# Performance work log

Hardware: AMD Instinct MI355X
Metric: run time of the kernel (lower is better)

## Reference

```python
import jax, jax.numpy as jnp
import numpy as np

N_NODES = 50000


def gcn_conv(x, W, b, src, dst, n_nodes):
    """PyG GCNConv: x' = D^-1/2 (A+I) D^-1/2 (x W) + b (symmetric norm, self-loops)."""
    h = x @ W  # [N, out]
    loop = jnp.arange(n_nodes, dtype=src.dtype)
    src_f = jnp.concatenate([src, loop])
    dst_f = jnp.concatenate([dst, loop])
    ones = jnp.ones(src_f.shape[0], dtype=h.dtype)
    deg = jax.ops.segment_sum(ones, dst_f, num_segments=n_nodes)
    dinv = jnp.where(deg > 0, jax.lax.rsqrt(deg), 0.0)
    norm = dinv[src_f] * dinv[dst_f]  # [E+N]
    msg = h[src_f] * norm[:, None]    # irregular gather over edges
    out = jax.ops.segment_sum(msg, dst_f, num_segments=n_nodes)
    return out + b


def setup_inputs() -> dict:
    key = jax.random.key(0)
    ks = jax.random.split(key, 9)
    d_in, d_h = 128, 128
    x = jax.random.normal(ks[0], (N_NODES, d_in), dtype=jnp.float32)
    edge_index = jax.random.randint(ks[1], (2, 800000), 0, N_NODES, dtype=jnp.int64)
    glorot = lambda k, fi, fo: jax.random.normal(k, (fi, fo), dtype=jnp.float32) * jnp.sqrt(2.0 / (fi + fo))
    return {
        "x": x,
        "edge_index": edge_index,
        "W1": glorot(ks[2], d_in, d_h), "b1": jnp.zeros((d_h,), jnp.float32),
        "W2": glorot(ks[3], d_h, d_h), "b2": jnp.zeros((d_h,), jnp.float32),
        "W3": glorot(ks[4], d_h, d_h), "b3": jnp.zeros((d_h,), jnp.float32),
    }


def reference(x, edge_index, W1, b1, W2, b2, W3, b3):
    src, dst = edge_index[0], edge_index[1]
    n = x.shape[0]
    h = jax.nn.relu(gcn_conv(x, W1, b1, src, dst, n))
    h = jax.nn.relu(gcn_conv(h, W2, b2, src, dst, n))
    h = gcn_conv(h, W3, b3, src, dst, n)
    return h
```

## Files before the change

kernel.cpp:

```cpp
#include <hip/hip_runtime.h>

#define N_NODES 50000
#define N_EDGES 800000
#define DIM 128
#define WT_BLOCKS 192
#define GEMM_BLOCKS ((N_NODES + 127) / 128)
#define NBUCKET ((N_NODES + 255) / 256)
#define P1_BLOCKS 200
#define P1_CHUNK 4000
#define P2_BLOCKS 200
#define P2_CHUNK 4000

typedef unsigned int u32;
typedef short bf16x8 __attribute__((ext_vector_type(8)));
typedef float f32x4 __attribute__((ext_vector_type(4)));

static inline size_t alignUp(size_t x) { return (x + 255) & ~size_t(255); }

__device__ inline unsigned short f2bf(float f) {
    union { float f; u32 u; } v; v.f = f;
    u32 r = v.u + 0x7fffu + ((v.u >> 16) & 1u);
    return (unsigned short)(r >> 16);
}
__device__ inline float bf_lo(u32 u) { return __uint_as_float(u << 16); }
__device__ inline float bf_hi(u32 u) { return __uint_as_float(u & 0xffff0000u); }

__global__ __launch_bounds__(256) void prep_kernel(const float* __restrict__ W1,
                                                   const float* __restrict__ W2,
                                                   const float* __restrict__ W3,
                                                   unsigned short* __restrict__ Wt,
                                                   const int* __restrict__ dst,
                                                   u32* __restrict__ bcnt) {
    __shared__ u32 hist[NBUCKET];
    int bid = blockIdx.x;
    if (bid < WT_BLOCKS) {
        int m = bid >> 6;
        int e = (bid & 63) * 256 + threadIdx.x;
        int n = e >> 7, k = e & 127;
        const float* W = (m == 0) ? W1 : (m == 1) ? W2 : W3;
        Wt[m * DIM * DIM + n * DIM + k] = f2bf(W[(size_t)k * DIM + n]);
        return;
    }
    int b = bid - WT_BLOCKS;
    for (int k = threadIdx.x; k < NBUCKET; k += 256) hist[k] = 0;
    __syncthreads();
    int e0 = b * P1_CHUNK;
    int e1 = min(e0 + P1_CHUNK, N_EDGES);
    for (int i = e0 + threadIdx.x; i < e1; i += 256)
        atomicAdd(&hist[((u32)dst[i]) >> 8], 1u);
    __syncthreads();
    for (int k = threadIdx.x; k < NBUCKET; k += 256)
        if (hist[k]) atomicAdd(&bcnt[k], hist[k]);
}

__global__ __launch_bounds__(256) void bscan_kernel(const u32* __restrict__ bcnt,
                                                    u32* __restrict__ bbase,
                                                    u32* __restrict__ bcur) {
    __shared__ u32 wsum[4];
    int tid = threadIdx.x, lane = tid & 63, wv = tid >> 6;
    u32 c = (tid < NBUCKET) ? bcnt[tid] : 0;
    u32 v = c;
#pragma unroll
    for (int off = 1; off < 64; off <<= 1) {
        u32 u = __shfl_up(v, off, 64);
        if (lane >= off) v += u;
    }
    if (lane == 63) wsum[wv] = v;
    __syncthreads();
    u32 wo = 0;
    for (int w = 0; w < wv; w++) wo += wsum[w];
    u32 excl = wo + v - c;
    if (tid < NBUCKET) { bbase[tid] = excl; bcur[tid] = excl; }
}

__global__ __launch_bounds__(256) void part_kernel(const int* __restrict__ src,
                                                   const int* __restrict__ dst,
                                                   u32* __restrict__ bcur,
                                                   u32* __restrict__ epart) {
    __shared__ u32 ed[P2_CHUNK];
    __shared__ u32 hist[NBUCKET];
    __shared__ u32 cb[NBUCKET];
    __shared__ u32 rk[NBUCKET];
    int tid = threadIdx.x;
    for (int k = tid; k < NBUCKET; k += 256) { hist[k] = 0; rk[k] = 0; }
    __syncthreads();
    int e0 = blockIdx.x * P2_CHUNK;
    int e1 = min(e0 + P2_CHUNK, N_EDGES);
    for (int i = e0 + tid; i < e1; i += 256) {
        u32 s = (u32)src[i], d = (u32)dst[i];
        u32 v = s | (d << 16);
        ed[i - e0] = v;
        atomicAdd(&hist[d >> 8], 1u);
    }
    __syncthreads();
    for (int k = tid; k < NBUCKET; k += 256) {
        u32 c = hist[k];
        cb[k] = c ? atomicAdd(&bcur[k], c) : 0u;
    }
    __syncthreads();
    int n = e1 - e0;
    for (int k = tid; k < n; k += 256) {
        u32 v = ed[k];
        u32 bk = v >> 24;
        u32 r = atomicAdd(&rk[bk], 1u);
        epart[cb[bk] + r] = v;
    }
}

#define LDSTRIDE 40
__global__ __launch_bounds__(256) void gemm_mfma_kernel(const float* __restrict__ x,
                                                        const unsigned short* __restrict__ xb,
                                                        const unsigned short* __restrict__ Wt,
                                                        unsigned short* __restrict__ hb,
                                                        int n_rows,
                                                        const u32* __restrict__ bbase,
                                                        const u32* __restrict__ bcnt,
                                                        const u32* __restrict__ epart,
                                                        int* __restrict__ cnt,
                                                        int* __restrict__ base,
                                                        float* __restrict__ dinv,
                                                        unsigned short* __restrict__ csr16) {
    __shared__ unsigned short As[128 * LDSTRIDE];
    __shared__ unsigned short Bs[128 * LDSTRIDE];
    if (blockIdx.x >= GEMM_BLOCKS) {
        int B = blockIdx.x - GEMM_BLOCKS;
        u32* hcnt = (u32*)&As[0];
        u32* pref = hcnt + 256;
        u32* wsum = pref + 256;
        int tid = threadIdx.x, lane = tid & 63, wv = tid >> 6;
        int nb0 = B << 8;
        u32 ebeg = bbase[B];
        u32 esz  = bcnt[B];
        hcnt[tid] = 0;
        __syncthreads();
        for (u32 k = tid; k < esz; k += 256)
            atomicAdd(&hcnt[(epart[ebeg + k] >> 16) & 255u], 1u);
        __syncthreads();
        u32 c = hcnt[tid];
        u32 v = c;
#pragma unroll
        for (int off = 1; off < 64; off <<= 1) {
            u32 u = __shfl_up(v, off, 64);
            if (lane >= off) v += u;
        }
        if (lane == 63) wsum[wv] = v;
        __syncthreads();
        u32 wo = 0;
        for (int w = 0; w < wv; w++) wo += wsum[w];
        u32 excl = wo + v - c;
        int node = nb0 + tid;
        if (node < N_NODES) {
            cnt[node]  = (int)c;
            base[node] = (int)(ebeg + excl);
            dinv[node] = rsqrtf((float)(c + 1));
        }
        pref[tid] = excl;
        __syncthreads();
        for (u32 k = tid; k < esz; k += 256) {
            u32 v2 = epart[ebeg + k];
            u32 dl = (v2 >> 16) & 255u;
            u32 r = atomicAdd(&pref[dl], 1u);
            csr16[ebeg + r] = (unsigned short)(v2 & 0xffffu);
        }
        return;
    }
    const int tid = threadIdx.x;
    const int wave = tid >> 6;
    const int lane = tid & 63;
    const int quad = lane >> 4;
    const int l16 = lane & 15;
    const int row0 = blockIdx.x * 128;

    f32x4 acc[2][8];
#pragma unroll
    for (int mt = 0; mt < 2; mt++)
#pragma unroll
        for (int nt = 0; nt < 8; nt++) acc[mt][nt] = (f32x4){0.f, 0.f, 0.f, 0.f};

    for (int k0 = 0; k0 < DIM; k0 += 32) {
        if (xb) {
#pragma unroll
            for (int p = 0; p < 2; p++) {
                int r = p * 64 + (tid >> 2);
                int kk = (tid & 3) * 8;
                int gr = row0 + r;
                uint4 v = make_uint4(0u, 0u, 0u, 0u);
                if (gr < n_rows) v = *(const uint4*)&xb[(size_t)gr * DIM + k0 + kk];
                *(uint4*)&As[r * LDSTRIDE + kk] = v;
            }
        } else {
#pragma unroll
            for (int p = 0; p < 4; p++) {
                int r = p * 32 + (tid >> 3);
                int kq = (tid & 7) * 4;
                int gr = row0 + r;
                float4 v = make_float4(0.f, 0.f, 0.f, 0.f);
                if (gr < n_rows) v = *(const float4*)&x[(size_t)gr * DIM + k0 + kq];
                u32 lo = (u32)f2bf(v.x) | ((u32)f2bf(v.y) << 16);
                u32 hi = (u32)f2bf(v.z) | ((u32)f2bf(v.w) << 16);
                *(uint2*)&As[r * LDSTRIDE + kq] = make_uint2(lo, hi);
            }
        }
#pragma unroll
        for (int p = 0; p < 2; p++) {
            int nn = p * 64 + (tid >> 2);
            int kk = (tid & 3) * 8;
            *(uint4*)&Bs[nn * LDSTRIDE + kk] = *(const uint4*)&Wt[nn * DIM + k0 + kk];
        }
        __syncthreads();
        const int m0 = wave * 32;
        bf16x8 a0 = *(const bf16x8*)&As[(m0 + l16) * LDSTRIDE + quad * 8];
        bf16x8 a1 = *(const bf16x8*)&As[(m0 + 16 + l16) * LDSTRIDE + quad * 8];
#pragma unroll
        for (int nt = 0; nt < 8; nt++) {
            bf16x8 b = *(const bf16x8*)&Bs[(nt * 16 + l16) * LDSTRIDE + quad * 8];
            acc[0][nt] = __builtin_amdgcn_mfma_f32_16x16x32_bf16(a0, b, acc[0][nt], 0, 0, 0);
            acc[1][nt] = __builtin_amdgcn_mfma_f32_16x16x32_bf16(a1, b, acc[1][nt], 0, 0, 0);
        }
        __syncthreads();
    }
    const int m0 = wave * 32;
#pragma unroll
    for (int mt = 0; mt < 2; mt++) {
#pragma unroll
        for (int reg = 0; reg < 4; reg++) {
            int gr = row0 + m0 + mt * 16 + quad * 4 + reg;
            if (gr < n_rows) {
#pragma unroll
                for (int nt = 0; nt < 8; nt++)
                    hb[(size_t)gr * DIM + nt * 16 + l16] = f2bf(acc[mt][nt][reg]);
            }
        }
    }
}

__device__ inline void accum8(float acc[8], uint4 r, float w) {
    acc[0] += w * bf_lo(r.x); acc[1] += w * bf_hi(r.x);
    acc[2] += w * bf_lo(r.y); acc[3] += w * bf_hi(r.y);
    acc[4] += w * bf_lo(r.z); acc[5] += w * bf_hi(r.z);
    acc[6] += w * bf_lo(r.w); acc[7] += w * bf_hi(r.w);
}

__global__ __launch_bounds__(256) void agg_kernel(const uint4* __restrict__ hb,
                                                  const int* __restrict__ cnt,
                                                  const int* __restrict__ basep,
                                                  const unsigned short* __restrict__ csr16,
                                                  const float* __restrict__ dinv,
                                                  const float4* __restrict__ bias4,
                                                  unsigned short* __restrict__ outb,
                                                  float* __restrict__ outf, int relu) {
    const int wave = threadIdx.x >> 6;
    const int lane = threadIdx.x & 63;
    const int node = blockIdx.x * 4 + wave;
    const int g = lane >> 4;
    const int l16 = lane & 15;

    const int deg = cnt[node];
    const float di = dinv[node];
    const int start = basep[node];

    float acc[8];
#pragma unroll
    for (int i = 0; i < 8; i++) acc[i] = 0.f;

    for (int b0 = 0; b0 < deg; b0 += 64) {
        int m = min(64, deg - b0);
        int e = 0; float w = 0.f;
        if (lane < m) {
            e = csr16[start + b0 + lane];
            w = dinv[e];
        }
        int j4 = 0;
        for (; j4 + 16 <= m; j4 += 16) {
            int j0 = j4 + g, j1 = j4 + 4 + g, j2 = j4 + 8 + g, j3 = j4 + 12 + g;
            int s0 = __shfl(e, j0, 64);  float w0 = __shfl(w, j0, 64);
            int s1 = __shfl(e, j1, 64);  float w1 = __shfl(w, j1, 64);
            int s2 = __shfl(e, j2, 64);  float w2 = __shfl(w, j2, 64);
            int s3 = __shfl(e, j3, 64);  float w3 = __shfl(w, j3, 64);
            uint4 r0 = hb[(size_t)s0 * 16 + l16];
            uint4 r1 = hb[(size_t)s1 * 16 + l16];
            uint4 r2 = hb[(size_t)s2 * 16 + l16];
            uint4 r3 = hb[(size_t)s3 * 16 + l16];
            accum8(acc, r0, w0);
            accum8(acc, r1, w1);
            accum8(acc, r2, w2);
            accum8(acc, r3, w3);
        }
        for (; j4 + 8 <= m; j4 += 8) {
            int j0 = j4 + g, j1 = j4 + 4 + g;
            int s0 = __shfl(e, j0, 64);  float w0 = __shfl(w, j0, 64);
            int s1 = __shfl(e, j1, 64);  float w1 = __shfl(w, j1, 64);
            uint4 r0 = hb[(size_t)s0 * 16 + l16];
            uint4 r1 = hb[(size_t)s1 * 16 + l16];
            accum8(acc, r0, w0);
            accum8(acc, r1, w1);
        }
        for (; j4 < m; j4 += 4) {
            int j = j4 + g;
            int jj = (j < m) ? j : 0;
            int s0 = __shfl(e, jj, 64);  float w0 = __shfl(w, jj, 64);
            if (j < m) {
                uint4 r0 = hb[(size_t)s0 * 16 + l16];
                accum8(acc, r0, w0);
            }
        }
    }
    if (g == 0) {
        uint4 r = hb[(size_t)node * 16 + l16];
        accum8(acc, r, di);
    }
#pragma unroll
    for (int i = 0; i < 8; i++) {
        acc[i] += __shfl_xor(acc[i], 16, 64);
        acc[i] += __shfl_xor(acc[i], 32, 64);
    }
    if (g == 0) {
        float4 b0 = bias4[l16 * 2], b1 = bias4[l16 * 2 + 1];
        float res[8];
        res[0] = di * acc[0] + b0.x; res[1] = di * acc[1] + b0.y;
        res[2] = di * acc[2] + b0.z; res[3] = di * acc[3] + b0.w;
        res[4] = di * acc[4] + b1.x; res[5] = di * acc[5] + b1.y;
        res[6] = di * acc[6] + b1.z; res[7] = di * acc[7] + b1.w;
        if (relu) {
#pragma unroll
            for (int i = 0; i < 8; i++) res[i] = fmaxf(res[i], 0.f);
        }
        if (outb) {
            u32 p0 = (u32)f2bf(res[0]) | ((u32)f2bf(res[1]) << 16);
            u32 p1 = (u32)f2bf(res[2]) | ((u32)f2bf(res[3]) << 16);
            u32 p2 = (u32)f2bf(res[4]) | ((u32)f2bf(res[5]) << 16);
            u32 p3 = (u32)f2bf(res[6]) | ((u32)f2bf(res[7]) << 16);
            ((uint4*)outb)[(size_t)node * 16 + l16] = make_uint4(p0, p1, p2, p3);
        } else {
            float4* o = (float4*)(outf + (size_t)node * DIM);
            o[l16 * 2]     = make_float4(res[0], res[1], res[2], res[3]);
            o[l16 * 2 + 1] = make_float4(res[4], res[5], res[6], res[7]);
        }
    }
}


extern "C" void kernel_launch(void* const* d_in, const int* in_sizes, int n_in,
                              void* d_out, int out_size, void* d_ws, size_t ws_size,
                              hipStream_t stream) {
    const float* x  = (const float*)d_in[0];
    const int* ei   = (const int*)d_in[1];
    const float* W1 = (const float*)d_in[2];
    const float* b1 = (const float*)d_in[3];
    const float* W2 = (const float*)d_in[4];
    const float* b2 = (const float*)d_in[5];
    const float* W3 = (const float*)d_in[6];
    const float* b3 = (const float*)d_in[7];
    const int* src = ei;
    const int* dst = ei + N_EDGES;
    float* out = (float*)d_out;

    char* w = (char*)d_ws;
    u32* bcnt  = (u32*)w; w += alignUp((size_t)NBUCKET * 4);
    u32* bbase = (u32*)w; w += alignUp((size_t)NBUCKET * 4);
    u32* bcur  = (u32*)w; w += alignUp((size_t)NBUCKET * 4);
    int* cnt   = (int*)w; w += alignUp((size_t)N_NODES * 4);
    int* base  = (int*)w; w += alignUp((size_t)N_NODES * 4);
    float* dinvb = (float*)w; w += alignUp((size_t)N_NODES * 4);
    u32* epart = (u32*)w; w += alignUp((size_t)N_EDGES * 4);
    unsigned short* csr16 = (unsigned short*)w; w += alignUp((size_t)N_EDGES * 2);
    unsigned short* wt = (unsigned short*)w; w += alignUp((size_t)3 * DIM * DIM * 2);
    unsigned short* hbuf = (unsigned short*)w; w += alignUp((size_t)N_NODES * DIM * 2);
    unsigned short* abuf = (unsigned short*)w; w += alignUp((size_t)N_NODES * DIM * 2);

    hipMemsetAsync(bcnt, 0, (size_t)NBUCKET * 4, stream);

    int ablocks = N_NODES / 4;

    prep_kernel<<<WT_BLOCKS + P1_BLOCKS, 256, 0, stream>>>(W1, W2, W3, wt, dst, bcnt);
    bscan_kernel<<<1, 256, 0, stream>>>(bcnt, bbase, bcur);
    part_kernel<<<P2_BLOCKS, 256, 0, stream>>>(src, dst, bcur, epart);

    gemm_mfma_kernel<<<GEMM_BLOCKS + NBUCKET, 256, 0, stream>>>(x, nullptr, wt, hbuf, N_NODES,
                                                                bbase, bcnt, epart,
                                                                cnt, base, dinvb, csr16);
    agg_kernel<<<ablocks, 256, 0, stream>>>((const uint4*)hbuf, cnt, base, csr16, dinvb,
                                            (const float4*)b1, abuf, nullptr, 1);

    gemm_mfma_kernel<<<GEMM_BLOCKS, 256, 0, stream>>>(nullptr, abuf, wt + DIM * DIM, hbuf,
                                                      N_NODES, nullptr, nullptr, nullptr,
                                                      nullptr, nullptr, nullptr, nullptr);
    agg_kernel<<<ablocks, 256, 0, stream>>>((const uint4*)hbuf, cnt, base, csr16, dinvb,
                                            (const float4*)b2, abuf, nullptr, 1);

    gemm_mfma_kernel<<<GEMM_BLOCKS, 256, 0, stream>>>(nullptr, abuf, wt + 2 * DIM * DIM, hbuf,
                                                      N_NODES, nullptr, nullptr, nullptr,
                                                      nullptr, nullptr, nullptr, nullptr);
    agg_kernel<<<ablocks, 256, 0, stream>>>((const uint4*)hbuf, cnt, base, csr16, dinvb,
                                            (const float4*)b3, nullptr, out, 0);
}
```

Before: 258.8 us.

## Fuse aggregation of layers 1-2 with the following layer's GEMM

Adds a fused kernel that aggregates 64 nodes per block into shared memory (bias, ReLU, bf16) and then multiplies them by the next layer's weights with MFMA. This replaces the separate agg and GEMM launches for layers 1 and 2, removing the write and re-read of the intermediate activation buffer and two kernel launches. The trade-off is fewer blocks (782 vs 12500), each wave processing 16 nodes serially. The extra LDS per block for the full weight tile may lower occupancy and latency hiding in the gather-bound aggregation.

```diff
diff --git a/kernel.cpp b/kernel.cpp
--- a/kernel.cpp
+++ b/kernel.cpp
@@ -5,6 +5,7 @@
 #define DIM 128
 #define WT_BLOCKS 192
 #define GEMM_BLOCKS ((N_NODES + 127) / 128)
+#define FUSE_BLOCKS ((N_NODES + 63) / 64)
 #define NBUCKET ((N_NODES + 255) / 256)
 #define P1_BLOCKS 200
 #define P1_CHUNK 4000
@@ -24,6 +25,13 @@
 }
 __device__ inline float bf_lo(u32 u) { return __uint_as_float(u << 16); }
 __device__ inline float bf_hi(u32 u) { return __uint_as_float(u & 0xffff0000u); }
+
+__device__ inline void accum8(float acc[8], uint4 r, float w) {
+    acc[0] += w * bf_lo(r.x); acc[1] += w * bf_hi(r.x);
+    acc[2] += w * bf_lo(r.y); acc[3] += w * bf_hi(r.y);
+    acc[4] += w * bf_lo(r.z); acc[5] += w * bf_hi(r.z);
+    acc[6] += w * bf_lo(r.w); acc[7] += w * bf_hi(r.w);
+}
 
 __global__ __launch_bounds__(256) void prep_kernel(const float* __restrict__ W1,
                                                    const float* __restrict__ W2,
@@ -109,7 +117,6 @@
 
 #define LDSTRIDE 40
 __global__ __launch_bounds__(256) void gemm_mfma_kernel(const float* __restrict__ x,
-                                                        const unsigned short* __restrict__ xb,
                                                         const unsigned short* __restrict__ Wt,
                                                         unsigned short* __restrict__ hb,
                                                         int n_rows,
@@ -178,28 +185,16 @@
         for (int nt = 0; nt < 8; nt++) acc[mt][nt] = (f32x4){0.f, 0.f, 0.f, 0.f};
 
     for (int k0 = 0; k0 < DIM; k0 += 32) {
-        if (xb) {
-#pragma unroll
-            for (int p = 0; p < 2; p++) {
-                int r = p * 64 + (tid >> 2);
-                int kk = (tid & 3) * 8;
-                int gr = row0 + r;
-                uint4 v = make_uint4(0u, 0u, 0u, 0u);
-                if (gr < n_rows) v = *(const uint4*)&xb[(size_t)gr * DIM + k0 + kk];
-                *(uint4*)&As[r * LDSTRIDE + kk] = v;
-            }
-        } else {
-#pragma unroll
-            for (int p = 0; p < 4; p++) {
-                int r = p * 32 + (tid >> 3);
-                int kq = (tid & 7) * 4;
-                int gr = row0 + r;
-                float4 v = make_float4(0.f, 0.f, 0.f, 0.f);
-                if (gr < n_rows) v = *(const float4*)&x[(size_t)gr * DIM + k0 + kq];
-                u32 lo = (u32)f2bf(v.x) | ((u32)f2bf(v.y) << 16);
-                u32 hi = (u32)f2bf(v.z) | ((u32)f2bf(v.w) << 16);
-                *(uint2*)&As[r * LDSTRIDE + kq] = make_uint2(lo, hi);
-            }
+#pragma unroll
+        for (int p = 0; p < 4; p++) {
+            int r = p * 32 + (tid >> 3);
+            int kq = (tid & 7) * 4;
+            int gr = row0 + r;
+            float4 v = make_float4(0.f, 0.f, 0.f, 0.f);
+            if (gr < n_rows) v = *(const float4*)&x[(size_t)gr * DIM + k0 + kq];
+            u32 lo = (u32)f2bf(v.x) | ((u32)f2bf(v.y) << 16);
+            u32 hi = (u32)f2bf(v.z) | ((u32)f2bf(v.w) << 16);
+            *(uint2*)&As[r * LDSTRIDE + kq] = make_uint2(lo, hi);
         }
 #pragma unroll
         for (int p = 0; p < 2; p++) {
@@ -234,11 +229,135 @@
     }
 }
 
-__device__ inline void accum8(float acc[8], uint4 r, float w) {
-    acc[0] += w * bf_lo(r.x); acc[1] += w * bf_hi(r.x);
-    acc[2] += w * bf_lo(r.y); acc[3] += w * bf_hi(r.y);
-    acc[4] += w * bf_lo(r.z); acc[5] += w * bf_hi(r.z);
-    acc[6] += w * bf_lo(r.w); acc[7] += w * bf_hi(r.w);
+#define FSTRIDE 136
+__global__ __launch_bounds__(256) void fused_agg_gemm_kernel(
+        const uint4* __restrict__ hb_in,
+        const unsigned short* __restrict__ Wt,
+        const int* __restrict__ cnt,
+        const int* __restrict__ basep,
+        const unsigned short* __restrict__ csr16,
+        const float* __restrict__ dinv,
+        const float4* __restrict__ bias4,
+        unsigned short* __restrict__ hb_out) {
+    __shared__ unsigned short As[64 * FSTRIDE];
+    __shared__ unsigned short Bs[128 * FSTRIDE];
+    const int tid = threadIdx.x;
+    const int wave = tid >> 6;
+    const int lane = tid & 63;
+    const int g = lane >> 4;
+    const int l16 = lane & 15;
+    const int row0 = blockIdx.x * 64;
+
+#pragma unroll
+    for (int i = 0; i < 8; i++) {
+        int idx = i * 256 + tid;
+        int n = idx >> 4, k8 = (idx & 15) * 8;
+        *(uint4*)&Bs[n * FSTRIDE + k8] = *(const uint4*)&Wt[n * DIM + k8];
+    }
+
+    for (int t = 0; t < 16; t++) {
+        const int lrow = wave * 16 + t;
+        const int node = row0 + lrow;
+        int deg = 0, start = 0;
+        float di = 0.f;
+        if (node < N_NODES) { deg = cnt[node]; start = basep[node]; di = dinv[node]; }
+
+        float acc[8];
+#pragma unroll
+        for (int i = 0; i < 8; i++) acc[i] = 0.f;
+
+        for (int b0 = 0; b0 < deg; b0 += 64) {
+            int m = min(64, deg - b0);
+            int e = 0; float w = 0.f;
+            if (lane < m) {
+                e = csr16[start + b0 + lane];
+                w = dinv[e];
+            }
+            int j4 = 0;
+            for (; j4 + 16 <= m; j4 += 16) {
+                int j0 = j4 + g, j1 = j4 + 4 + g, j2 = j4 + 8 + g, j3 = j4 + 12 + g;
+                int s0 = __shfl(e, j0, 64);  float w0 = __shfl(w, j0, 64);
+                int s1 = __shfl(e, j1, 64);  float w1 = __shfl(w, j1, 64);
+                int s2 = __shfl(e, j2, 64);  float w2 = __shfl(w, j2, 64);
+                int s3 = __shfl(e, j3, 64);  float w3 = __shfl(w, j3, 64);
+                uint4 r0 = hb_in[(size_t)s0 * 16 + l16];
+                uint4 r1 = hb_in[(size_t)s1 * 16 + l16];
+                uint4 r2 = hb_in[(size_t)s2 * 16 + l16];
+                uint4 r3 = hb_in[(size_t)s3 * 16 + l16];
+                accum8(acc, r0, w0);
+                accum8(acc, r1, w1);
+                accum8(acc, r2, w2);
+                accum8(acc, r3, w3);
+            }
+            for (; j4 + 8 <= m; j4 += 8) {
+                int j0 = j4 + g, j1 = j4 + 4 + g;
+                int s0 = __shfl(e, j0, 64);  float w0 = __shfl(w, j0, 64);
+                int s1 = __shfl(e, j1, 64);  float w1 = __shfl(w, j1, 64);
+                uint4 r0 = hb_in[(size_t)s0 * 16 + l16];
+                uint4 r1 = hb_in[(size_t)s1 * 16 + l16];
+                accum8(acc, r0, w0);
+                accum8(acc, r1, w1);
+            }
+            for (; j4 < m; j4 += 4) {
+                int j = j4 + g;
+                int jj = (j < m) ? j : 0;
+                int s0 = __shfl(e, jj, 64);  float w0 = __shfl(w, jj, 64);
+                if (j < m) {
+                    uint4 r0 = hb_in[(size_t)s0 * 16 + l16];
+                    accum8(acc, r0, w0);
+                }
+            }
+        }
+        if (g == 0 && node < N_NODES) {
+            uint4 r = hb_in[(size_t)node * 16 + l16];
+            accum8(acc, r, di);
+        }
+#pragma unroll
+        for (int i = 0; i < 8; i++) {
+            acc[i] += __shfl_xor(acc[i], 16, 64);
+            acc[i] += __shfl_xor(acc[i], 32, 64);
+        }
+        if (g == 0) {
+            float4 bv0 = bias4[l16 * 2], bv1 = bias4[l16 * 2 + 1];
+            float res[8];
+            res[0] = di * acc[0] + bv0.x; res[1] = di * acc[1] + bv0.y;
+            res[2] = di * acc[2] + bv0.z; res[3] = di * acc[3] + bv0.w;
+            res[4] = di * acc[4] + bv1.x; res[5] = di * acc[5] + bv1.y;
+            res[6] = di * acc[6] + bv1.z; res[7] = di * acc[7] + bv1.w;
+#pragma unroll
+            for (int i = 0; i < 8; i++) res[i] = fmaxf(res[i], 0.f);
+            u32 p0 = (u32)f2bf(res[0]) | ((u32)f2bf(res[1]) << 16);
+            u32 p1 = (u32)f2bf(res[2]) | ((u32)f2bf(res[3]) << 16);
+            u32 p2 = (u32)f2bf(res[4]) | ((u32)f2bf(res[5]) << 16);
+            u32 p3 = (u32)f2bf(res[6]) | ((u32)f2bf(res[7]) << 16);
+            *(uint4*)&As[lrow * FSTRIDE + l16 * 8] = make_uint4(p0, p1, p2, p3);
+        }
+    }
+    __syncthreads();
+
+    const int quad = g;
+    const int w16 = wave * 16;
+    f32x4 gacc[8];
+#pragma unroll
+    for (int nt = 0; nt < 8; nt++) gacc[nt] = (f32x4){0.f, 0.f, 0.f, 0.f};
+#pragma unroll
+    for (int ks = 0; ks < 4; ks++) {
+        bf16x8 a = *(const bf16x8*)&As[(w16 + l16) * FSTRIDE + ks * 32 + quad * 8];
+#pragma unroll
+        for (int nt = 0; nt < 8; nt++) {
+            bf16x8 b = *(const bf16x8*)&Bs[(nt * 16 + l16) * FSTRIDE + ks * 32 + quad * 8];
+            gacc[nt] = __builtin_amdgcn_mfma_f32_16x16x32_bf16(a, b, gacc[nt], 0, 0, 0);
+        }
+    }
+#pragma unroll
+    for (int reg = 0; reg < 4; reg++) {
+        int gr = row0 + w16 + quad * 4 + reg;
+        if (gr < N_NODES) {
+#pragma unroll
+            for (int nt = 0; nt < 8; nt++)
+                hb_out[(size_t)gr * DIM + nt * 16 + l16] = f2bf(gacc[nt][reg]);
+        }
+    }
 }
 
 __global__ __launch_bounds__(256) void agg_kernel(const uint4* __restrict__ hb,
@@ -247,8 +366,7 @@
                                                   const unsigned short* __restrict__ csr16,
                                                   const float* __restrict__ dinv,
                                                   const float4* __restrict__ bias4,
-                                                  unsigned short* __restrict__ outb,
-                                                  float* __restrict__ outf, int relu) {
+                                                  float* __restrict__ out) {
     const int wave = threadIdx.x >> 6;
     const int lane = threadIdx.x & 63;
     const int node = blockIdx.x * 4 + wave;
@@ -316,26 +434,11 @@
     }
     if (g == 0) {
         float4 b0 = bias4[l16 * 2], b1 = bias4[l16 * 2 + 1];
-        float res[8];
-        res[0] = di * acc[0] + b0.x; res[1] = di * acc[1] + b0.y;
-        res[2] = di * acc[2] + b0.z; res[3] = di * acc[3] + b0.w;
-        res[4] = di * acc[4] + b1.x; res[5] = di * acc[5] + b1.y;
-        res[6] = di * acc[6] + b1.z; res[7] = di * acc[7] + b1.w;
-        if (relu) {
-#pragma unroll
-            for (int i = 0; i < 8; i++) res[i] = fmaxf(res[i], 0.f);
-        }
-        if (outb) {
-            u32 p0 = (u32)f2bf(res[0]) | ((u32)f2bf(res[1]) << 16);
-            u32 p1 = (u32)f2bf(res[2]) | ((u32)f2bf(res[3]) << 16);
-            u32 p2 = (u32)f2bf(res[4]) | ((u32)f2bf(res[5]) << 16);
-            u32 p3 = (u32)f2bf(res[6]) | ((u32)f2bf(res[7]) << 16);
-            ((uint4*)outb)[(size_t)node * 16 + l16] = make_uint4(p0, p1, p2, p3);
-        } else {
-            float4* o = (float4*)(outf + (size_t)node * DIM);
-            o[l16 * 2]     = make_float4(res[0], res[1], res[2], res[3]);
-            o[l16 * 2 + 1] = make_float4(res[4], res[5], res[6], res[7]);
-        }
+        float4* o = (float4*)(out + (size_t)node * DIM);
+        o[l16 * 2]     = make_float4(di * acc[0] + b0.x, di * acc[1] + b0.y,
+                                     di * acc[2] + b0.z, di * acc[3] + b0.w);
+        o[l16 * 2 + 1] = make_float4(di * acc[4] + b1.x, di * acc[5] + b1.y,
+                                     di * acc[6] + b1.z, di * acc[7] + b1.w);
     }
 }
 
@@ -365,32 +468,24 @@
     u32* epart = (u32*)w; w += alignUp((size_t)N_EDGES * 4);
     unsigned short* csr16 = (unsigned short*)w; w += alignUp((size_t)N_EDGES * 2);
     unsigned short* wt = (unsigned short*)w; w += alignUp((size_t)3 * DIM * DIM * 2);
-    unsigned short* hbuf = (unsigned short*)w; w += alignUp((size_t)N_NODES * DIM * 2);
-    unsigned short* abuf = (unsigned short*)w; w += alignUp((size_t)N_NODES * DIM * 2);
+    unsigned short* hbuf  = (unsigned short*)w; w += alignUp((size_t)N_NODES * DIM * 2);
+    unsigned short* hbuf2 = (unsigned short*)w; w += alignUp((size_t)N_NODES * DIM * 2);
 
     hipMemsetAsync(bcnt, 0, (size_t)NBUCKET * 4, stream);
-
-    int ablocks = N_NODES / 4;
 
     prep_kernel<<<WT_BLOCKS + P1_BLOCKS, 256, 0, stream>>>(W1, W2, W3, wt, dst, bcnt);
     bscan_kernel<<<1, 256, 0, stream>>>(bcnt, bbase, bcur);
     part_kernel<<<P2_BLOCKS, 256, 0, stream>>>(src, dst, bcur, epart);
 
-    gemm_mfma_kernel<<<GEMM_BLOCKS + NBUCKET, 256, 0, stream>>>(x, nullptr, wt, hbuf, N_NODES,
+    gemm_mfma_kernel<<<GEMM_BLOCKS + NBUCKET, 256, 0, stream>>>(x, wt, hbuf, N_NODES,
                                                                 bbase, bcnt, epart,
                                                                 cnt, base, dinvb, csr16);
-    agg_kernel<<<ablocks, 256, 0, stream>>>((const uint4*)hbuf, cnt, base, csr16, dinvb,
-                                            (const float4*)b1, abuf, nullptr, 1);
-
-    gemm_mfma_kernel<<<GEMM_BLOCKS, 256, 0, stream>>>(nullptr, abuf, wt + DIM * DIM, hbuf,
-                                                      N_NODES, nullptr, nullptr, nullptr,
-                                                      nullptr, nullptr, nullptr, nullptr);
-    agg_kernel<<<ablocks, 256, 0, stream>>>((const uint4*)hbuf, cnt, base, csr16, dinvb,
-                                            (const float4*)b2, abuf, nullptr, 1);
-
-    gemm_mfma_kernel<<<GEMM_BLOCKS, 256, 0, stream>>>(nullptr, abuf, wt + 2 * DIM * DIM, hbuf,
-                                                      N_NODES, nullptr, nullptr, nullptr,
-                                                      nullptr, nullptr, nullptr, nullptr);
-    agg_kernel<<<ablocks, 256, 0, stream>>>((const uint4*)hbuf, cnt, base, csr16, dinvb,
-                                            (const float4*)b3, nullptr, out, 0);
-}
+    fused_agg_gemm_kernel<<<FUSE_BLOCKS, 256, 0, stream>>>((const uint4*)hbuf, wt + DIM * DIM,
+                                                           cnt, base, csr16, dinvb,
+                                                           (const float4*)b1, hbuf2);
+    fused_agg_gemm_kernel<<<FUSE_BLOCKS, 256, 0, stream>>>((const uint4*)hbuf2, wt + 2 * DIM * DIM,
+                                                           cnt, base, csr16, dinvb,
+                                                           (const float4*)b2, hbuf);
+    agg_kernel<<<N_NODES / 4, 256, 0, stream>>>((const uint4*)hbuf, cnt, base, csr16, dinvb,
+                                                (const float4*)b3, out);
+}
```

Measured after the change: 338.0 us. +30.6%, slower.
